# Kernel optimization log

Hardware: AMD Instinct MI355X
Metric: run time of the kernel (lower is better)

## Reference

```python
import jax, jax.numpy as jnp
import numpy as np

N_NODES = 50000
N_EDGES = 800000
D_IN = 788
D_HID = 256
N_REL = 7
N_CLS = 2


def rgcn_conv(x, w_rel, w_root, b, src, dst, edge_type):
    """PyG RGCNConv with default mean aggregation per relation + root weight + bias.
    x: (N, F_in); w_rel: (R, F_in, F_out); w_root: (F_in, F_out); b: (F_out,).
    src/dst: (E,) with edge_index[0]=source j, edge_index[1]=target i.
    """
    R, _, F_out = w_rel.shape
    N = x.shape[0]
    # transform-then-gather (equivalent to PyG's gather-then-transform, cheaper)
    x_rel = jnp.einsum('nf,rfo->rno', x, w_rel)          # (R, N, F_out)
    msg = x_rel[edge_type, src]                           # (E, F_out)
    agg = jnp.zeros((R, N, F_out), x.dtype).at[edge_type, dst].add(msg)
    cnt = jnp.zeros((R, N), x.dtype).at[edge_type, dst].add(1.0)
    out = (agg / jnp.clip(cnt, 1.0)[..., None]).sum(0)    # mean per relation, summed over relations
    return out + x @ w_root + b


def setup_inputs() -> dict:
    key = jax.random.key(0)
    ks = jax.random.split(key, 9)
    x = jax.random.normal(ks[0], (N_NODES, D_IN), dtype=jnp.float32)
    edge_index = jax.random.randint(ks[1], (2, N_EDGES), 0, N_NODES, dtype=jnp.int64)
    edge_type = jax.random.randint(ks[2], (N_EDGES,), 0, N_REL, dtype=jnp.int64)
    s1 = 0.05
    w1_rel = jax.random.normal(ks[3], (N_REL, D_IN, D_HID), dtype=jnp.float32) * s1
    w1_root = jax.random.normal(ks[4], (D_IN, D_HID), dtype=jnp.float32) * s1
    b1 = jnp.zeros((D_HID,), dtype=jnp.float32)
    w2_rel = jax.random.normal(ks[5], (N_REL, D_HID, N_CLS), dtype=jnp.float32) * s1
    w2_root = jax.random.normal(ks[6], (D_HID, N_CLS), dtype=jnp.float32) * s1
    b2 = jnp.zeros((N_CLS,), dtype=jnp.float32)
    return {"x": x, "edge_index": edge_index, "edge_type": edge_type,
            "w1_rel": w1_rel, "w1_root": w1_root, "b1": b1,
            "w2_rel": w2_rel, "w2_root": w2_root, "b2": b2}


def reference(x, edge_index, edge_type, w1_rel, w1_root, b1, w2_rel, w2_root, b2):
    src, dst = edge_index[0], edge_index[1]
    h = jax.nn.relu(rgcn_conv(x, w1_rel, w1_root, b1, src, dst, edge_type))
    # F.dropout(p=0.5) is identity in eval mode
    out = rgcn_conv(h, w2_rel, w2_root, b2, src, dst, edge_type)
    return out
```

## Files before the change

kernel.cpp:

```cpp
#include <hip/hip_runtime.h>
#include <hip/hip_bf16.h>
#include <stdint.h>

#define N_NODES 50000
#define N_EDGES 800000
#define D_IN    788
#define D_INP   800
#define D_HID   256
#define N_REL   7
#define NBINS   (N_REL * N_NODES)
#define NSCANB  342
#define NXTILE  391

typedef __attribute__((ext_vector_type(8))) short bf16x8;
typedef __attribute__((ext_vector_type(4))) float f32x4;
typedef __attribute__((ext_vector_type(4))) unsigned int u32x4;

__device__ __forceinline__ unsigned short f2bf(float f) {
  union { __hip_bfloat16 h; unsigned short u; } v;
  v.h = __float2bfloat16(f);
  return v.u;
}

__device__ __forceinline__ f32x4 bf4(ushort4 g) {
  union { unsigned int u; float f; } a, b, c, d;
  a.u = (unsigned)g.x << 16; b.u = (unsigned)g.y << 16;
  c.u = (unsigned)g.z << 16; d.u = (unsigned)g.w << 16;
  return (f32x4){a.f, b.f, c.f, d.f};
}

#define GLOAD16(g, l) __builtin_amdgcn_global_load_lds(                      \
    (const __attribute__((address_space(1))) unsigned int*)(g),              \
    (__attribute__((address_space(3))) unsigned int*)(l), 16, 0, 0)

__global__ void k_conv_w(const float* __restrict__ w_rel, const float* __restrict__ w_root,
                         unsigned short* __restrict__ wt) {
  int t = blockIdx.x * blockDim.x + threadIdx.x;
  if (t >= 8 * D_HID * 100) return;
  int m = t / (D_HID * 100);
  int rem = t % (D_HID * 100);
  int o = rem / 100, gi = rem % 100;
  int chunk = gi >> 2, p = gi & 3;
  int g = p ^ ((o >> 1) & 3);
  int k0 = chunk * 32 + g * 8;
  const float* src = (m < N_REL) ? (w_rel + (size_t)m * D_IN * D_HID) : w_root;
  union { unsigned short us[8]; u32x4 v; } pk;
#pragma unroll
  for (int j = 0; j < 8; j++)
    pk.us[j] = (k0 + j < D_IN) ? f2bf(src[(size_t)(k0 + j) * D_HID + o]) : (unsigned short)0;
  *(u32x4*)(wt + (size_t)(m * D_HID + o) * D_INP + chunk * 32 + p * 8) = pk.v;
}

__global__ void k_xbf(const float* __restrict__ x, unsigned short* __restrict__ xb) {
  int t = blockIdx.x * blockDim.x + threadIdx.x;
  if (t >= N_NODES * 100) return;
  int n = t / 100, gi = t % 100;
  int chunk = gi >> 2, p = gi & 3;
  int g = p ^ ((n >> 1) & 3);
  int c = chunk * 32 + g * 8;
  union { unsigned short us[8]; u32x4 v; } pk;
  if (c + 7 < D_IN) {
    float4 a = *(const float4*)(x + (size_t)n * D_IN + c);
    float4 b = *(const float4*)(x + (size_t)n * D_IN + c + 4);
    pk.us[0] = f2bf(a.x); pk.us[1] = f2bf(a.y); pk.us[2] = f2bf(a.z); pk.us[3] = f2bf(a.w);
    pk.us[4] = f2bf(b.x); pk.us[5] = f2bf(b.y); pk.us[6] = f2bf(b.z); pk.us[7] = f2bf(b.w);
  } else {
#pragma unroll
    for (int j = 0; j < 8; j++)
      pk.us[j] = (c + j < D_IN) ? f2bf(x[(size_t)n * D_IN + c + j]) : (unsigned short)0;
  }
  *(u32x4*)(xb + (size_t)n * D_INP + chunk * 32 + p * 8) = pk.v;
}

__global__ void k_count(const int* __restrict__ etype, const int* __restrict__ edst,
                        int* __restrict__ cnt) {
  int t = blockIdx.x * blockDim.x + threadIdx.x;
  if (t >= N_EDGES) return;
  atomicAdd(&cnt[etype[t] * N_NODES + edst[t]], 1);
}

__global__ void k_scan1(const int* __restrict__ cnt, int* __restrict__ bsum) {
  __shared__ int wsh[4];
  int b = blockIdx.x, tid = threadIdx.x;
  int base = b * 1024 + tid * 4;
  int4 v = {0, 0, 0, 0};
  if (base + 3 < NBINS) v = *(const int4*)(cnt + base);
  else { for (int i = 0; i < 4; i++) if (base + i < NBINS) ((int*)&v)[i] = cnt[base + i]; }
  int s = v.x + v.y + v.z + v.w;
  for (int o = 32; o > 0; o >>= 1) s += __shfl_down(s, o);
  if ((tid & 63) == 0) wsh[tid >> 6] = s;
  __syncthreads();
  if (tid == 0) bsum[b] = wsh[0] + wsh[1] + wsh[2] + wsh[3];
}

__global__ void k_scan2(const int* __restrict__ bsum, int* __restrict__ boff) {
  __shared__ int tmp[512];
  int tid = threadIdx.x;
  int mine = (tid < NSCANB) ? bsum[tid] : 0;
  tmp[tid] = mine;
  __syncthreads();
  for (int o = 1; o < 512; o <<= 1) {
    int v = (tid >= o) ? tmp[tid - o] : 0;
    __syncthreads();
    tmp[tid] += v;
    __syncthreads();
  }
  if (tid < NSCANB) boff[tid] = tmp[tid] - mine;
}

__global__ void k_scan3(const int* __restrict__ cnt, const int* __restrict__ boff,
                        int* __restrict__ S) {
  __shared__ int wsum[4];
  int b = blockIdx.x, tid = threadIdx.x;
  int base = b * 1024 + tid * 4;
  int4 v = {0, 0, 0, 0};
  if (base + 3 < NBINS) v = *(const int4*)(cnt + base);
  else { for (int i = 0; i < 4; i++) if (base + i < NBINS) ((int*)&v)[i] = cnt[base + i]; }
  int s = v.x + v.y + v.z + v.w;
  int lane = tid & 63, w = tid >> 6;
  int sc = s;
  for (int o = 1; o < 64; o <<= 1) { int u = __shfl_up(sc, o); if (lane >= o) sc += u; }
  if (lane == 63) wsum[w] = sc;
  __syncthreads();
  int wbase = 0;
  for (int i = 0; i < w; i++) wbase += wsum[i];
  int excl = boff[b] + wbase + sc - s;
  int o0 = excl, o1 = excl + v.x, o2 = o1 + v.y, o3 = o2 + v.z;
  if (base + 3 < NBINS) { int4 o4 = {o0, o1, o2, o3}; *(int4*)(S + base) = o4; }
  else {
    if (base     < NBINS) S[base]     = o0;
    if (base + 1 < NBINS) S[base + 1] = o1;
    if (base + 2 < NBINS) S[base + 2] = o2;
    if (base + 3 < NBINS) S[base + 3] = o3;
  }
}

__global__ void k_scatter(const int* __restrict__ etype, const int* __restrict__ edst,
                          const int* __restrict__ esrc, const int* __restrict__ S,
                          int* __restrict__ rank, int* __restrict__ psrc) {
  int t = blockIdx.x * blockDim.x + threadIdx.x;
  if (t >= N_EDGES) return;
  int bin = etype[t] * N_NODES + edst[t];
  int r = atomicAdd(&rank[bin], 1);
  psrc[S[bin] + r] = esrc[t];
}

template<int SWZ, int NMAT>
__global__ __launch_bounds__(512) void k_gemm_g(
    const unsigned short* __restrict__ xb, const unsigned short* __restrict__ wt,
    unsigned short* __restrict__ xrs, int mb) {
  __shared__ __align__(16) unsigned short As[128 * 32];
  __shared__ __align__(16) unsigned short Bs[256 * 32];

  int tid = threadIdx.x;
  int bx, by;
  if (SWZ) {
    int b = blockIdx.x;
    int l = (b % 8) * (NXTILE * NMAT / 8) + b / 8;
    bx = l / NMAT; by = l % NMAT;
  } else {
    bx = blockIdx.x; by = blockIdx.y;
  }
  int mat = mb + by;
  int m0 = bx * 128;
  const unsigned short* wsec = wt + (size_t)mat * (D_HID * D_INP);
  int lane = tid & 63, w = tid >> 6;
  int wm = w >> 2, wn = w & 3;

  int ar = tid >> 2;
  int arow = m0 + ar; if (arow > N_NODES - 1) arow = N_NODES - 1;
  const unsigned short* asrc = xb + (size_t)arow * D_INP + (tid & 3) * 8;
  const unsigned short* bsrc0 = wsec + (size_t)(tid >> 2) * D_INP + (tid & 3) * 8;
  const unsigned short* bsrc1 = bsrc0 + (size_t)128 * D_INP;
  unsigned short* al = As + tid * 8;
  unsigned short* bl0 = Bs + tid * 8;
  unsigned short* bl1 = Bs + 4096 + tid * 8;

  f32x4 acc[4][4];
#pragma unroll
  for (int i = 0; i < 4; i++)
#pragma unroll
    for (int j = 0; j < 4; j++) acc[i][j] = (f32x4){0.f, 0.f, 0.f, 0.f};

  int row = lane & 15, quad = lane >> 4;
  int rg = (quad ^ ((row >> 1) & 3)) * 8;

  for (int ks = 0; ks < 25; ks++) {
    int ko = ks * 32;
    GLOAD16(asrc + ko, al);
    GLOAD16(bsrc0 + ko, bl0);
    GLOAD16(bsrc1 + ko, bl1);
    __syncthreads();

    bf16x8 af[4], bfr[4];
#pragma unroll
    for (int i = 0; i < 4; i++)
      af[i] = *(const bf16x8*)(As + (wm * 64 + i * 16 + row) * 32 + rg);
#pragma unroll
    for (int j = 0; j < 4; j++)
      bfr[j] = *(const bf16x8*)(Bs + (wn * 64 + j * 16 + row) * 32 + rg);
#pragma unroll
    for (int i = 0; i < 4; i++)
#pragma unroll
      for (int j = 0; j < 4; j++)
        acc[i][j] = __builtin_amdgcn_mfma_f32_16x16x32_bf16(af[i], bfr[j], acc[i][j], 0, 0, 0);
    __syncthreads();
  }

  int col_l = lane & 15, rquad = lane >> 4;
  unsigned short* xo = xrs + (size_t)by * ((size_t)N_NODES * D_HID);
#pragma unroll
  for (int i = 0; i < 4; i++) {
#pragma unroll
    for (int reg = 0; reg < 4; reg++) {
      int node = m0 + wm * 64 + i * 16 + rquad * 4 + reg;
      if (node < N_NODES) {
#pragma unroll
        for (int j = 0; j < 4; j++)
          xo[(size_t)node * D_HID + wn * 64 + j * 16 + col_l] = f2bf(acc[i][j][reg]);
      }
    }
  }
}

__global__ __launch_bounds__(256) void k_gemm_f(
    const float* __restrict__ x, const unsigned short* __restrict__ wt,
    unsigned short* __restrict__ xrs, int mb) {
  __shared__ __align__(16) unsigned short As[64 * 40];
  __shared__ __align__(16) unsigned short Bs[256 * 40];

  int tid = threadIdx.x;
  int mat = mb + blockIdx.y;
  int m0 = blockIdx.x * 64;
  const unsigned short* wsec = wt + (size_t)mat * (D_HID * D_INP);
  int lane = tid & 63, w = tid >> 6;

  int ra = tid >> 2, ca = tid & 3, ca8 = ca * 8;
  int arow = m0 + ra; if (arow > N_NODES - 1) arow = N_NODES - 1;
  const float* apf = x + (size_t)arow * D_IN;
  const unsigned short* bgp = wsec + (size_t)ra * D_INP + (ca ^ ((ra >> 1) & 3)) * 8;
  unsigned short* al = As + ra * 40 + ca8;
  unsigned short* bl = Bs + ra * 40 + ca8;

  f32x4 acc[4][4];
#pragma unroll
  for (int i = 0; i < 4; i++)
#pragma unroll
    for (int j = 0; j < 4; j++) acc[i][j] = (f32x4){0.f, 0.f, 0.f, 0.f};

  float4 pa0 = *(const float4*)(apf + ca8);
  float4 pa1 = *(const float4*)(apf + ca8 + 4);
  u32x4 pb0 = *(const u32x4*)(bgp);
  u32x4 pb1 = *(const u32x4*)(bgp +  64 * D_INP);
  u32x4 pb2 = *(const u32x4*)(bgp + 128 * D_INP);
  u32x4 pb3 = *(const u32x4*)(bgp + 192 * D_INP);

  int row = lane & 15, quad = lane >> 4;
  for (int ks = 0; ks < 25; ks++) {
    if (ks < 24) {
      union { unsigned short us[8]; u32x4 v; } pk;
      pk.us[0] = f2bf(pa0.x); pk.us[1] = f2bf(pa0.y);
      pk.us[2] = f2bf(pa0.z); pk.us[3] = f2bf(pa0.w);
      pk.us[4] = f2bf(pa1.x); pk.us[5] = f2bf(pa1.y);
      pk.us[6] = f2bf(pa1.z); pk.us[7] = f2bf(pa1.w);
      *(u32x4*)al = pk.v;
    } else {
      float v0 = pa0.x, v1 = pa0.y, v2 = pa0.z, v3 = pa0.w;
      float v4 = pa1.x, v5 = pa1.y, v6 = pa1.z, v7 = pa1.w;
      if (ca8 == 16) { v0 = pa1.x; v1 = pa1.y; v2 = pa1.z; v3 = pa1.w;
                       v4 = 0.f; v5 = 0.f; v6 = 0.f; v7 = 0.f; }
      if (ca8 == 24) { v0 = 0.f; v1 = 0.f; v2 = 0.f; v3 = 0.f;
                       v4 = 0.f; v5 = 0.f; v6 = 0.f; v7 = 0.f; }
      union { unsigned short us[8]; u32x4 v; } pk;
      pk.us[0] = f2bf(v0); pk.us[1] = f2bf(v1); pk.us[2] = f2bf(v2); pk.us[3] = f2bf(v3);
      pk.us[4] = f2bf(v4); pk.us[5] = f2bf(v5); pk.us[6] = f2bf(v6); pk.us[7] = f2bf(v7);
      *(u32x4*)al = pk.v;
    }
    *(u32x4*)bl = pb0;
    *(u32x4*)(bl +  64 * 40) = pb1;
    *(u32x4*)(bl + 128 * 40) = pb2;
    *(u32x4*)(bl + 192 * 40) = pb3;
    __syncthreads();

    if (ks < 24) {
      int on = (ks + 1) * 32 + ca8;
      int lo = (on > 780) ? 780 : on;
      pa0 = *(const float4*)(apf + lo);
      pa1 = *(const float4*)(apf + lo + 4);
      int ko = (ks + 1) * 32;
      pb0 = *(const u32x4*)(bgp + ko);
      pb1 = *(const u32x4*)(bgp + ko +  64 * D_INP);
      pb2 = *(const u32x4*)(bgp + ko + 128 * D_INP);
      pb3 = *(const u32x4*)(bgp + ko + 192 * D_INP);
    }

    bf16x8 af[4], bfr[4];
#pragma unroll
    for (int i = 0; i < 4; i++)
      af[i] = *(const bf16x8*)(As + (i * 16 + row) * 40 + quad * 8);
#pragma unroll
    for (int j = 0; j < 4; j++)
      bfr[j] = *(const bf16x8*)(Bs + (w * 64 + j * 16 + row) * 40 + quad * 8);
#pragma unroll
    for (int i = 0; i < 4; i++)
#pragma unroll
      for (int j = 0; j < 4; j++)
        acc[i][j] = __builtin_amdgcn_mfma_f32_16x16x32_bf16(af[i], bfr[j], acc[i][j], 0, 0, 0);
    __syncthreads();
  }

  int col_l = lane & 15, rquad = lane >> 4;
  unsigned short* xo = xrs + (size_t)blockIdx.y * ((size_t)N_NODES * D_HID);
#pragma unroll
  for (int i = 0; i < 4; i++) {
#pragma unroll
    for (int reg = 0; reg < 4; reg++) {
      int node = m0 + i * 16 + rquad * 4 + reg;
      if (node < N_NODES) {
#pragma unroll
        for (int j = 0; j < 4; j++)
          xo[(size_t)node * D_HID + w * 64 + j * 16 + col_l] = f2bf(acc[i][j][reg]);
      }
    }
  }
}

__global__ __launch_bounds__(256) void k_agg8(
    const unsigned short* __restrict__ xrs, const int* __restrict__ S,
    const int* __restrict__ cnt, const int* __restrict__ psrc,
    const float* __restrict__ b1, const float* __restrict__ w2rel,
    const float* __restrict__ w2root, float* __restrict__ y) {
  __shared__ float hsh[4][256];
  int wv = threadIdx.x >> 6;
  int n = blockIdx.x * 4 + wv;
  int lane = threadIdx.x & 63;
  if (n >= N_NODES) return;

  int c_l = 0, p_l = 0;
  if (lane < N_REL) {
    c_l = cnt[lane * N_NODES + n];
    p_l = S[lane * N_NODES + n];
  }

  f32x4 acc = (f32x4){0.f, 0.f, 0.f, 0.f};
#pragma unroll
  for (int r = 0; r < N_REL; r++) {
    int c = __shfl(c_l, r);
    if (c > 0) {
      int p = __shfl(p_l, r);
      const unsigned short* slab = xrs + (size_t)r * N_NODES * D_HID;
      f32x4 s = (f32x4){0.f, 0.f, 0.f, 0.f};
      int e = 0;
      for (; e + 1 < c; e += 2) {
        int s0 = psrc[p + e], s1 = psrc[p + e + 1];
        ushort4 g0 = *(const ushort4*)(slab + (size_t)s0 * D_HID + lane * 4);
        ushort4 g1 = *(const ushort4*)(slab + (size_t)s1 * D_HID + lane * 4);
        s += bf4(g0) + bf4(g1);
      }
      if (e < c) {
        int s0 = psrc[p + e];
        ushort4 g0 = *(const ushort4*)(slab + (size_t)s0 * D_HID + lane * 4);
        s += bf4(g0);
      }
      acc += s * (1.0f / (float)c);
    }
  }

  ushort4 gr = *(const ushort4*)(xrs + ((size_t)7 * N_NODES + n) * D_HID + lane * 4);
  acc += bf4(gr);
  f32x4 b = *(const f32x4*)(b1 + lane * 4);
  f32x4 hv;
  hv[0] = fmaxf(acc[0] + b[0], 0.f);
  hv[1] = fmaxf(acc[1] + b[1], 0.f);
  hv[2] = fmaxf(acc[2] + b[2], 0.f);
  hv[3] = fmaxf(acc[3] + b[3], 0.f);

  *(f32x4*)&hsh[wv][lane * 4] = hv;
  __builtin_amdgcn_wave_barrier();

  int m = lane >> 3, sl = lane & 7;
  const float* wp = (m < N_REL) ? (w2rel + m * (D_HID * 2)) : w2root;
  float d0 = 0.f, d1 = 0.f;
#pragma unroll
  for (int j = 0; j < 8; j++) {
    int db = sl * 4 + j * 32;
    f32x4 h4 = *(const f32x4*)&hsh[wv][db];
    f32x4 wa = *(const f32x4*)(wp + db * 2);
    f32x4 wb = *(const f32x4*)(wp + db * 2 + 4);
    d0 += h4[0] * wa[0] + h4[1] * wa[2] + h4[2] * wb[0] + h4[3] * wb[2];
    d1 += h4[0] * wa[1] + h4[1] * wa[3] + h4[2] * wb[1] + h4[3] * wb[3];
  }
  d0 += __shfl_down(d0, 1); d1 += __shfl_down(d1, 1);
  d0 += __shfl_down(d0, 2); d1 += __shfl_down(d1, 2);
  d0 += __shfl_down(d0, 4); d1 += __shfl_down(d1, 4);
  if (sl == 0) {
    y[(size_t)m * (N_NODES * 2) + n * 2]     = d0;
    y[(size_t)m * (N_NODES * 2) + n * 2 + 1] = d1;
  }
}

__global__ __launch_bounds__(256) void k_agg(
    const unsigned short* __restrict__ xrs, const int* __restrict__ S,
    const int* __restrict__ cnt, const int* __restrict__ psrc,
    float* __restrict__ h, const float* __restrict__ b1,
    const float* __restrict__ w2rel, const float* __restrict__ w2root,
    float* __restrict__ y, int r0, int pass) {
  int n = blockIdx.x * 4 + (threadIdx.x >> 6);
  int lane = threadIdx.x & 63;
  if (n >= N_NODES) return;
  f32x4 acc;
  if (pass == 0) acc = (f32x4){0.f, 0.f, 0.f, 0.f};
  else acc = *(const f32x4*)(h + (size_t)n * D_HID + lane * 4);

  int nr = (pass < 3) ? 2 : 1;
  for (int rr = 0; rr < nr; rr++) {
    int bin = (r0 + rr) * N_NODES + n;
    int c = cnt[bin];
    if (c > 0) {
      int p = S[bin];
      f32x4 s = (f32x4){0.f, 0.f, 0.f, 0.f};
      int e = 0;
      for (; e + 1 < c; e += 2) {
        int s0 = psrc[p + e], s1 = psrc[p + e + 1];
        ushort4 g0 = *(const ushort4*)(xrs + ((size_t)rr * N_NODES + s0) * D_HID + lane * 4);
        ushort4 g1 = *(const ushort4*)(xrs + ((size_t)rr * N_NODES + s1) * D_HID + lane * 4);
        s += bf4(g0) + bf4(g1);
      }
      if (e < c) {
        int s0 = psrc[p + e];
        ushort4 g0 = *(const ushort4*)(xrs + ((size_t)rr * N_NODES + s0) * D_HID + lane * 4);
        s += bf4(g0);
      }
      acc += s * (1.0f / (float)c);
    }
  }

  if (pass < 3) {
    *(f32x4*)(h + (size_t)n * D_HID + lane * 4) = acc;
    return;
  }

  ushort4 gr = *(const ushort4*)(xrs + ((size_t)1 * N_NODES + n) * D_HID + lane * 4);
  acc += bf4(gr);
  f32x4 b = *(const f32x4*)(b1 + lane * 4);
  f32x4 hv;
  hv[0] = fmaxf(acc[0] + b[0], 0.f);
  hv[1] = fmaxf(acc[1] + b[1], 0.f);
  hv[2] = fmaxf(acc[2] + b[2], 0.f);
  hv[3] = fmaxf(acc[3] + b[3], 0.f);

#pragma unroll
  for (int m = 0; m < 8; m++) {
    const float* wp = (m < N_REL) ? (w2rel + m * (D_HID * 2)) : w2root;
    f32x4 wa = *(const f32x4*)(wp + lane * 8);
    f32x4 wb = *(const f32x4*)(wp + lane * 8 + 4);
    float d0 = hv[0] * wa[0] + hv[1] * wa[2] + hv[2] * wb[0] + hv[3] * wb[2];
    float d1 = hv[0] * wa[1] + hv[1] * wa[3] + hv[2] * wb[1] + hv[3] * wb[3];
#pragma unroll
    for (int off = 32; off > 0; off >>= 1) {
      d0 += __shfl_down(d0, off);
      d1 += __shfl_down(d1, off);
    }
    if (lane == 0) {
      y[(size_t)m * (N_NODES * 2) + n * 2]     = d0;
      y[(size_t)m * (N_NODES * 2) + n * 2 + 1] = d1;
    }
  }
}

__global__ void k_out(const float* __restrict__ y, const float* __restrict__ b2,
                      const int* __restrict__ cnt, const int* __restrict__ S,
                      const int* __restrict__ psrc, float* __restrict__ out) {
  int t = blockIdx.x * blockDim.x + threadIdx.x;
  if (t < NBINS) {
    int c = cnt[t];
    if (c == 0) return;
    int p = S[t];
    int r = t / N_NODES;
    int i = t - r * N_NODES;
    const float* yr = y + (size_t)r * (N_NODES * 2);
    float s0 = 0.f, s1 = 0.f;
    for (int e = 0; e < c; e++) {
      int sc = psrc[p + e];
      float2 v = *(const float2*)(yr + sc * 2);
      s0 += v.x; s1 += v.y;
    }
    float is = 1.0f / (float)c;
    atomicAdd(out + (size_t)i * 2,     s0 * is);
    atomicAdd(out + (size_t)i * 2 + 1, s1 * is);
  } else if (t < NBINS + N_NODES) {
    int i = t - NBINS;
    float2 v = *(const float2*)(y + (size_t)N_REL * (N_NODES * 2) + i * 2);
    atomicAdd(out + (size_t)i * 2,     v.x + b2[0]);
    atomicAdd(out + (size_t)i * 2 + 1, v.y + b2[1]);
  }
}

#define OFF_WT   0u
#define OFF_XRS  3276800u
#define OFF_H    54476800u
#define OFF_CNT  105676800u
#define OFF_RANK 107076800u
#define OFF_S    108476800u
#define OFF_PSRC 109876800u
#define OFF_Y    113076800u
#define OFF_BSUM 116276800u
#define OFF_BOFF 116278848u
#define OFF_XB   116280896u
#define WS_NEED_XB 196280896ull

#define F_OFF_WT   0u
#define F_OFF_XRS  3276800u
#define F_OFF_CNT  208076800u
#define F_OFF_RANK 209476800u
#define F_OFF_S    210876800u
#define F_OFF_PSRC 212276800u
#define F_OFF_Y    215476800u
#define F_OFF_BSUM 218676800u
#define F_OFF_BOFF 218678848u
#define F_OFF_XB   218680896u
#define WS_NEED_FULL 298680896ull

extern "C" void kernel_launch(void* const* d_in, const int* in_sizes, int n_in,
                              void* d_out, int out_size, void* d_ws, size_t ws_size,
                              hipStream_t stream) {
  const float* x      = (const float*)d_in[0];
  const int*   eidx   = (const int*)d_in[1];
  const int*   etype  = (const int*)d_in[2];
  const float* w1rel  = (const float*)d_in[3];
  const float* w1root = (const float*)d_in[4];
  const float* b1     = (const float*)d_in[5];
  const float* w2rel  = (const float*)d_in[6];
  const float* w2root = (const float*)d_in[7];
  const float* b2     = (const float*)d_in[8];
  float* out = (float*)d_out;
  char* ws = (char*)d_ws;
  const int* esrc = eidx;
  const int* edst = eidx + N_EDGES;

  const bool full = (ws_size >= WS_NEED_FULL);
  const bool big  = !full && (ws_size >= WS_NEED_XB);

  hipMemsetAsync(d_out, 0, (size_t)out_size * sizeof(float), stream);

  if (full) {
    unsigned short* wt  = (unsigned short*)(ws + F_OFF_WT);
    unsigned short* xrs = (unsigned short*)(ws + F_OFF_XRS);
    int*   cnt  = (int*)(ws + F_OFF_CNT);
    int*   rank = (int*)(ws + F_OFF_RANK);
    int*   S    = (int*)(ws + F_OFF_S);
    int*   psrc = (int*)(ws + F_OFF_PSRC);
    float* y    = (float*)(ws + F_OFF_Y);
    int*   bsum = (int*)(ws + F_OFF_BSUM);
    int*   boff = (int*)(ws + F_OFF_BOFF);
    unsigned short* xb = (unsigned short*)(ws + F_OFF_XB);

    hipMemsetAsync(ws + F_OFF_CNT, 0, 2800000u, stream);

    k_conv_w<<<(8 * D_HID * 100 + 255) / 256, 256, 0, stream>>>(w1rel, w1root, wt);
    k_xbf<<<(N_NODES * 100 + 255) / 256, 256, 0, stream>>>(x, xb);
    k_count<<<(N_EDGES + 255) / 256, 256, 0, stream>>>(etype, edst, cnt);
    k_scan1<<<NSCANB, 256, 0, stream>>>(cnt, bsum);
    k_scan2<<<1, 512, 0, stream>>>(bsum, boff);
    k_scan3<<<NSCANB, 256, 0, stream>>>(cnt, boff, S);
    k_scatter<<<(N_EDGES + 255) / 256, 256, 0, stream>>>(etype, edst, esrc, S, rank, psrc);

    k_gemm_g<1, 8><<<NXTILE * 8, 512, 0, stream>>>(xb, wt, xrs, 0);
    k_agg8<<<(N_NODES + 3) / 4, 256, 0, stream>>>(xrs, S, cnt, psrc,
                                                  b1, w2rel, w2root, y);
    k_out<<<(NBINS + N_NODES + 255) / 256, 256, 0, stream>>>(y, b2, cnt, S, psrc, out);
    return;
  }

  unsigned short* wt  = (unsigned short*)(ws + OFF_WT);
  unsigned short* xrs = (unsigned short*)(ws + OFF_XRS);
  float* h    = (float*)(ws + OFF_H);
  int*   cnt  = (int*)(ws + OFF_CNT);
  int*   rank = (int*)(ws + OFF_RANK);
  int*   S    = (int*)(ws + OFF_S);
  int*   psrc = (int*)(ws + OFF_PSRC);
  float* y    = (float*)(ws + OFF_Y);
  int*   bsum = (int*)(ws + OFF_BSUM);
  int*   boff = (int*)(ws + OFF_BOFF);
  unsigned short* xb = (unsigned short*)(ws + OFF_XB);

  hipMemsetAsync(ws + OFF_CNT, 0, 2800000u, stream);

  k_conv_w<<<(8 * D_HID * 100 + 255) / 256, 256, 0, stream>>>(w1rel, w1root, wt);
  if (big)
    k_xbf<<<(N_NODES * 100 + 255) / 256, 256, 0, stream>>>(x, xb);
  k_count<<<(N_EDGES + 255) / 256, 256, 0, stream>>>(etype, edst, cnt);
  k_scan1<<<NSCANB, 256, 0, stream>>>(cnt, bsum);
  k_scan2<<<1, 512, 0, stream>>>(bsum, boff);
  k_scan3<<<NSCANB, 256, 0, stream>>>(cnt, boff, S);
  k_scatter<<<(N_EDGES + 255) / 256, 256, 0, stream>>>(etype, edst, esrc, S, rank, psrc);

  for (int p = 0; p < 4; p++) {
    if (big)
      k_gemm_g<0, 2><<<dim3(NXTILE, 2), 512, 0, stream>>>(xb, wt, xrs, 2 * p);
    else
      k_gemm_f<<<dim3(782, 2), 256, 0, stream>>>(x, wt, xrs, 2 * p);
    k_agg<<<(N_NODES + 3) / 4, 256, 0, stream>>>(xrs, S, cnt, psrc, h,
                                                 b1, w2rel, w2root, y, 2 * p, p);
  }

  k_out<<<(NBINS + N_NODES + 255) / 256, 256, 0, stream>>>(y, b2, cnt, S, psrc, out);
}
```

Measured before the change: 704.2 us.

## Double-buffer GEMM LDS tiles and coalesce weight conversion kernel

```diff
diff --git a/kernel.cpp b/kernel.cpp
--- a/kernel.cpp
+++ b/kernel.cpp
@@ -35,20 +35,28 @@
 
 __global__ void k_conv_w(const float* __restrict__ w_rel, const float* __restrict__ w_root,
                          unsigned short* __restrict__ wt) {
-  int t = blockIdx.x * blockDim.x + threadIdx.x;
-  if (t >= 8 * D_HID * 100) return;
-  int m = t / (D_HID * 100);
-  int rem = t % (D_HID * 100);
-  int o = rem / 100, gi = rem % 100;
-  int chunk = gi >> 2, p = gi & 3;
-  int g = p ^ ((o >> 1) & 3);
-  int k0 = chunk * 32 + g * 8;
+  int b = blockIdx.x;
+  int m = b / 25, chunk = b % 25;
+  int o = threadIdx.x;
   const float* src = (m < N_REL) ? (w_rel + (size_t)m * D_IN * D_HID) : w_root;
-  union { unsigned short us[8]; u32x4 v; } pk;
-#pragma unroll
-  for (int j = 0; j < 8; j++)
-    pk.us[j] = (k0 + j < D_IN) ? f2bf(src[(size_t)(k0 + j) * D_HID + o]) : (unsigned short)0;
-  *(u32x4*)(wt + (size_t)(m * D_HID + o) * D_INP + chunk * 32 + p * 8) = pk.v;
+  int k0 = chunk * 32;
+
+  unsigned short v[32];
+#pragma unroll
+  for (int kk = 0; kk < 32; kk++) {
+    int k = k0 + kk;
+    v[kk] = (k < D_IN) ? f2bf(src[(size_t)k * D_HID + o]) : (unsigned short)0;
+  }
+
+  unsigned short* dst = wt + ((size_t)m * D_HID + o) * D_INP + chunk * 32;
+  int sw = (o >> 1) & 3;
+#pragma unroll
+  for (int g = 0; g < 4; g++) {
+    union { unsigned short us[8]; u32x4 u; } pk;
+#pragma unroll
+    for (int j = 0; j < 8; j++) pk.us[j] = v[g * 8 + j];
+    *(u32x4*)(dst + (g ^ sw) * 8) = pk.u;
+  }
 }
 
 __global__ void k_xbf(const float* __restrict__ x, unsigned short* __restrict__ xb) {
@@ -149,8 +157,8 @@
 __global__ __launch_bounds__(512) void k_gemm_g(
     const unsigned short* __restrict__ xb, const unsigned short* __restrict__ wt,
     unsigned short* __restrict__ xrs, int mb) {
-  __shared__ __align__(16) unsigned short As[128 * 32];
-  __shared__ __align__(16) unsigned short Bs[256 * 32];
+  __shared__ __align__(16) unsigned short As[2][128 * 32];
+  __shared__ __align__(16) unsigned short Bs[2][256 * 32];
 
   int tid = threadIdx.x;
   int bx, by;
@@ -172,9 +180,6 @@
   const unsigned short* asrc = xb + (size_t)arow * D_INP + (tid & 3) * 8;
   const unsigned short* bsrc0 = wsec + (size_t)(tid >> 2) * D_INP + (tid & 3) * 8;
   const unsigned short* bsrc1 = bsrc0 + (size_t)128 * D_INP;
-  unsigned short* al = As + tid * 8;
-  unsigned short* bl0 = Bs + tid * 8;
-  unsigned short* bl1 = Bs + 4096 + tid * 8;
 
   f32x4 acc[4][4];
 #pragma unroll
@@ -185,26 +190,37 @@
   int row = lane & 15, quad = lane >> 4;
   int rg = (quad ^ ((row >> 1) & 3)) * 8;
 
+  GLOAD16(asrc,  &As[0][0] + tid * 8);
+  GLOAD16(bsrc0, &Bs[0][0] + tid * 8);
+  GLOAD16(bsrc1, &Bs[0][0] + 4096 + tid * 8);
+  __syncthreads();
+
+  int cur = 0;
   for (int ks = 0; ks < 25; ks++) {
-    int ko = ks * 32;
-    GLOAD16(asrc + ko, al);
-    GLOAD16(bsrc0 + ko, bl0);
-    GLOAD16(bsrc1 + ko, bl1);
-    __syncthreads();
-
+    if (ks < 24) {
+      int ko = (ks + 1) * 32;
+      GLOAD16(asrc + ko,  &As[cur ^ 1][0] + tid * 8);
+      GLOAD16(bsrc0 + ko, &Bs[cur ^ 1][0] + tid * 8);
+      GLOAD16(bsrc1 + ko, &Bs[cur ^ 1][0] + 4096 + tid * 8);
+    }
+
+    const unsigned short* Ac = &As[cur][0];
+    const unsigned short* Bc = &Bs[cur][0];
     bf16x8 af[4], bfr[4];
 #pragma unroll
     for (int i = 0; i < 4; i++)
-      af[i] = *(const bf16x8*)(As + (wm * 64 + i * 16 + row) * 32 + rg);
+      af[i] = *(const bf16x8*)(Ac + (wm * 64 + i * 16 + row) * 32 + rg);
 #pragma unroll
     for (int j = 0; j < 4; j++)
-      bfr[j] = *(const bf16x8*)(Bs + (wn * 64 + j * 16 + row) * 32 + rg);
+      bfr[j] = *(const bf16x8*)(Bc + (wn * 64 + j * 16 + row) * 32 + rg);
 #pragma unroll
     for (int i = 0; i < 4; i++)
 #pragma unroll
       for (int j = 0; j < 4; j++)
         acc[i][j] = __builtin_amdgcn_mfma_f32_16x16x32_bf16(af[i], bfr[j], acc[i][j], 0, 0, 0);
+
     __syncthreads();
+    cur ^= 1;
   }
 
   int col_l = lane & 15, rquad = lane >> 4;
@@ -557,7 +573,7 @@
 
     hipMemsetAsync(ws + F_OFF_CNT, 0, 2800000u, stream);
 
-    k_conv_w<<<(8 * D_HID * 100 + 255) / 256, 256, 0, stream>>>(w1rel, w1root, wt);
+    k_conv_w<<<8 * 25, 256, 0, stream>>>(w1rel, w1root, wt);
     k_xbf<<<(N_NODES * 100 + 255) / 256, 256, 0, stream>>>(x, xb);
     k_count<<<(N_EDGES + 255) / 256, 256, 0, stream>>>(etype, edst, cnt);
     k_scan1<<<NSCANB, 256, 0, stream>>>(cnt, bsum);
@@ -586,7 +602,7 @@
 
   hipMemsetAsync(ws + OFF_CNT, 0, 2800000u, stream);
 
-  k_conv_w<<<(8 * D_HID * 100 + 255) / 256, 256, 0, stream>>>(w1rel, w1root, wt);
+  k_conv_w<<<8 * 25, 256, 0, stream>>>(w1rel, w1root, wt);
   if (big)
     k_xbf<<<(N_NODES * 100 + 255) / 256, 256, 0, stream>>>(x, xb);
   k_count<<<(N_EDGES + 255) / 256, 256, 0, stream>>>(etype, edst, cnt);
```

Measured after the change: 711.9 us. About the same (+1.1%).
